# Kernel tuning notes

Measured on AMD Instinct MI355X. Metric: run time of the kernel, lower is better.

The kernel has to match this reference:

```python
import jax, jax.numpy as jnp
import numpy as np

B, H, W = 32768, 28, 28
HID = 800


def dft2(x):
    # centered 2D DFT: fftshift(fft2(ifftshift(x)))
    ax = (-2, -1)
    return jnp.fft.fftshift(jnp.fft.fft2(jnp.fft.ifftshift(x, axes=ax), axes=ax), axes=ax)


def idft2(x):
    ax = (-2, -1)
    return jnp.fft.fftshift(jnp.fft.ifft2(jnp.fft.ifftshift(x, axes=ax), axes=ax), axes=ax)


def setup_inputs() -> dict:
    key = jax.random.key(0)
    k = jax.random.split(key, 5)
    x = jax.random.normal(k[0], (B, H, W), dtype=jnp.float32)
    tmask_re = jnp.ones((1, H, W), dtype=jnp.float32)
    tmask_im = jnp.zeros((1, H, W), dtype=jnp.float32)
    w1 = jax.random.normal(k[1], (HID, H * W), dtype=jnp.float32) * 0.03
    b1 = jax.random.normal(k[2], (HID,), dtype=jnp.float32) * 0.03
    w4 = jax.random.normal(k[3], (10, HID), dtype=jnp.float32) * 0.03
    b4 = jax.random.normal(k[4], (10,), dtype=jnp.float32) * 0.03
    return {"x": x, "tmask_re": tmask_re, "tmask_im": tmask_im,
            "w1": w1, "b1": b1, "w4": w4, "b4": b4}


def reference(x, tmask_re, tmask_im, w1, b1, w4, b4):
    tmask = jax.lax.complex(tmask_re, tmask_im)          # [1,28,28] complex64
    xf = dft2(x.astype(jnp.complex64))                    # [B,28,28] complex64
    xf = tmask * xf                                       # elementwise complex mask
    xr = jnp.real(idft2(xf))                              # back to real image
    h = xr.reshape(-1, H * W)                             # [B,784]
    h = jax.nn.relu(h @ w1.T + b1)                        # [B,800]
    logits = h @ w4.T + b4                                # [B,10]
    return jax.nn.log_softmax(logits, axis=-1)
```

## Files before the change

kernel.cpp:

```cpp
#include <hip/hip_runtime.h>
#include <hip/hip_bf16.h>
#include <cmath>

typedef unsigned short u16;
typedef __attribute__((ext_vector_type(8))) short short8v;
typedef __attribute__((ext_vector_type(4))) unsigned short ushort4v;
typedef __attribute__((ext_vector_type(8))) unsigned short ushort8v;
typedef __attribute__((ext_vector_type(4))) float f32x4;

#define NPIX 784
#define KP   800
#define NH   800
#define STRIDE 808

__device__ __forceinline__ u16 f2bf(float f) {
    union { float f; unsigned int u; } v; v.f = f;
    unsigned int u = v.u;
    unsigned int r = (u + 0x7FFFu + ((u >> 16) & 1u)) >> 16;
    return (u16)r;
}

__global__ void k_kre(const float* __restrict__ MRE, const float* __restrict__ MIM,
                      float* __restrict__ KRE, float* __restrict__ FLAG)
{
    __shared__ float msre[784], msim[784], tre[784], tim[784];
    __shared__ float c28[28], s28[28];
    __shared__ int smax;

    const int t = threadIdx.x;
    if (t < 28) {
        float th = (float)t * (6.283185307179586f / 28.0f);
        s28[t] = sinf(th);
        c28[t] = cosf(th);
    }
    if (t == 0) smax = 0;
    if (t < 784) {
        int r = t / 28, c = t - r * 28;
        int idx = ((r + 14) % 28) * 28 + ((c + 14) % 28);
        msre[t] = MRE[idx];
        msim[t] = MIM[idx];
    }
    __syncthreads();
    if (t < 784) {
        int u = t / 28, cc = t - u * 28;
        float re = 0.f, im = 0.f;
        int ph = 0;
        for (int v = 0; v < 28; ++v) {
            float cr = c28[ph], ci = s28[ph];
            float ar = msre[u * 28 + v], ai = msim[u * 28 + v];
            re += ar * cr - ai * ci;
            im += ar * ci + ai * cr;
            ph += cc; if (ph >= 28) ph -= 28;
        }
        tre[t] = re; tim[t] = im;
    }
    __syncthreads();
    float dev = 0.f;
    if (t < 784) {
        int pr = t / 28, pc = t - pr * 28;
        float s = 0.f;
        int ph = 0;
        for (int u = 0; u < 28; ++u) {
            s += tre[u * 28 + pc] * c28[ph] - tim[u * 28 + pc] * s28[ph];
            ph += pr; if (ph >= 28) ph -= 28;
        }
        s *= (1.0f / 784.0f);
        KRE[t] = s;
        dev = fabsf(s - (t == 0 ? 1.0f : 0.0f));
    }
    #pragma unroll
    for (int m = 32; m >= 1; m >>= 1) dev = fmaxf(dev, __shfl_xor(dev, m, 64));
    if ((t & 63) == 0) atomicMax(&smax, __float_as_int(dev));
    __syncthreads();
    if (t == 0) FLAG[0] = (__int_as_float(smax) < 1e-4f) ? 1.0f : 0.0f;
}

__global__ void k_w1pack(const float* __restrict__ W1, const float* __restrict__ KRE,
                         const float* __restrict__ FLAG, u16* __restrict__ W1P)
{
    const int c = blockIdx.x;
    const int t = threadIdx.x;
    const bool delta = (FLAG[0] > 0.5f);
    __shared__ float w1d[56 * 56];
    __shared__ float kr[784];

    if (delta) {
        if (t < 100) {
            int k0 = t * 8;
            ushort8v h;
            if (k0 + 7 < NPIX) {
                const float4* wp = (const float4*)(W1 + (size_t)c * NPIX + k0);
                float4 a = wp[0], b = wp[1];
                h[0] = f2bf(a.x); h[1] = f2bf(a.y); h[2] = f2bf(a.z); h[3] = f2bf(a.w);
                h[4] = f2bf(b.x); h[5] = f2bf(b.y); h[6] = f2bf(b.z); h[7] = f2bf(b.w);
            } else {
                #pragma unroll
                for (int e = 0; e < 8; ++e) {
                    int k = k0 + e;
                    h[e] = (k < NPIX) ? f2bf(W1[(size_t)c * NPIX + k]) : (u16)0;
                }
            }
            int kf = k0 >> 5, r = k0 & 31;
            int l  = ((r >> 3) << 4) | (c & 15);
            int nf = c >> 4;
            ((ushort8v*)W1P)[(nf * 25 + kf) * 64 + l] = h;
        }
        return;
    }
    for (int i = t; i < 784; i += 128) kr[i] = KRE[i];
    for (int i = t; i < 3136; i += 128) {
        int r = i / 56, cc = i - r * 56;
        w1d[i] = W1[(size_t)c * NPIX + (r % 28) * 28 + (cc % 28)];
    }
    __syncthreads();
    for (int k = t; k < KP; k += 128) {
        float v = 0.f;
        if (k < NPIX) {
            int krr = k / 28, kcc = k - krr * 28;
            for (int dr = 0; dr < 28; ++dr) {
                const float* wrow = &w1d[(krr + dr) * 56 + kcc];
                const float* krow = &kr[dr * 28];
                #pragma unroll 4
                for (int dc = 0; dc < 28; ++dc) v += wrow[dc] * krow[dc];
            }
        }
        int kf = k >> 5, r = k & 31;
        int l  = ((r >> 3) << 4) | (c & 15);
        int nf = c >> 4;
        W1P[(size_t)(((nf * 25 + kf) * 64 + l) << 3) | (r & 7)] = f2bf(v);
    }
}

__global__ void k_w4pack(const float* __restrict__ W4, u16* __restrict__ W4P)
{
    int i = blockIdx.x * 256 + threadIdx.x;
    if (i >= 1600) return;
    int l = i & 63, kt = i >> 6;
    int lc = l & 15, lk = l >> 4;
    ushort8v h;
    #pragma unroll
    for (int e = 0; e < 8; ++e) {
        int k = kt * 32 + lk * 8 + e;
        h[e] = (lc < 10) ? f2bf(W4[lc * NH + k]) : (u16)0;
    }
    ((ushort8v*)W4P)[i] = h;
}

__global__ __launch_bounds__(640) __attribute__((amdgpu_waves_per_eu(3, 3)))
void k_main(
    const float* __restrict__ X, const u16* __restrict__ W1P,
    const u16* __restrict__ W4P, const float* __restrict__ B1,
    const float* __restrict__ B4, float* __restrict__ OUT)
{
    __shared__ __align__(16) u16 As[64 * STRIDE];
    __shared__ __align__(16) float PL2[10 * 4 * 64 * 4];

    const int t = threadIdx.x;
    const int row0 = blockIdx.x * 64;
    const int l = t & 63, w = t >> 6;
    const int lc = l & 15, lk = l >> 4;

    #pragma unroll
    for (int pass = 0; pass < 2; ++pass) {
        float4 y[10];
        #pragma unroll
        for (int i = 0; i < 10; ++i) {
            int idx = t + 640 * (pass * 10 + i);
            int row = idx / 200, q = idx - row * 200;
            if (q < 196)
                y[i] = *(const float4*)(X + (size_t)(row0 + row) * NPIX + (q << 2));
            else
                y[i] = make_float4(0.f, 0.f, 0.f, 0.f);
        }
        #pragma unroll
        for (int i = 0; i < 10; ++i) {
            int idx = t + 640 * (pass * 10 + i);
            int row = idx / 200, q = idx - row * 200;
            ushort4v h;
            h[0] = f2bf(y[i].x); h[1] = f2bf(y[i].y);
            h[2] = f2bf(y[i].z); h[3] = f2bf(y[i].w);
            *(ushort4v*)(As + row * STRIDE + (q << 2)) = h;
        }
    }

    f32x4 acc[4][5];
    #pragma unroll
    for (int m = 0; m < 4; ++m)
        #pragma unroll
        for (int n = 0; n < 5; ++n) acc[m][n] = (f32x4)(0.0f);

    const short8v* BP = (const short8v*)W1P;
    short8v bb[2][5];
    #pragma unroll
    for (int n = 0; n < 5; ++n)
        bb[0][n] = BP[((w * 5 + n) * 25 + 0) * 64 + l];

    __syncthreads();

    #pragma unroll
    for (int kt = 0; kt < 25; ++kt) {
        if (kt < 24) {
            #pragma unroll
            for (int n = 0; n < 5; ++n)
                bb[(kt + 1) & 1][n] = BP[((w * 5 + n) * 25 + (kt + 1)) * 64 + l];
        }
        const u16* ab = As + lc * STRIDE + kt * 32 + lk * 8;
        __builtin_amdgcn_s_setprio(1);
        #pragma unroll
        for (int m = 0; m < 4; ++m) {
            short8v a = *(const short8v*)(ab + m * (16 * STRIDE));
            #pragma unroll
            for (int n = 0; n < 5; ++n)
                acc[m][n] = __builtin_amdgcn_mfma_f32_16x16x32_bf16(a, bb[kt & 1][n], acc[m][n], 0, 0, 0);
        }
        __builtin_amdgcn_s_setprio(0);
    }
    __syncthreads();

    #pragma unroll
    for (int n = 0; n < 5; ++n) {
        float bn = B1[w * 80 + n * 16 + lc];
        #pragma unroll
        for (int m = 0; m < 4; ++m) {
            #pragma unroll
            for (int j = 0; j < 4; ++j) {
                float hv = fmaxf(acc[m][n][j] + bn, 0.0f);
                As[(m * 16 + lk * 4 + j) * STRIDE + (w * 80 + n * 16 + lc)] = f2bf(hv);
            }
        }
    }
    __syncthreads();

    {
        const int ks  = (w < 5) ? 3 * w : 15 + 2 * (w - 5);
        const int cnt = (w < 5) ? 3 : 2;
        const short8v* WP = (const short8v*)W4P;
        f32x4 pc[4];
        #pragma unroll
        for (int m = 0; m < 4; ++m) pc[m] = (f32x4)(0.0f);
        #pragma unroll
        for (int i = 0; i < 3; ++i) {
            if (i < cnt) {
                int kt = ks + i;
                short8v b = WP[kt * 64 + l];
                #pragma unroll
                for (int m = 0; m < 4; ++m) {
                    short8v a = *(const short8v*)(As + (m * 16 + lc) * STRIDE + kt * 32 + lk * 8);
                    pc[m] = __builtin_amdgcn_mfma_f32_16x16x32_bf16(a, b, pc[m], 0, 0, 0);
                }
            }
        }
        f32x4* PLv = (f32x4*)PL2;
        #pragma unroll
        for (int m = 0; m < 4; ++m)
            PLv[(w * 4 + m) * 64 + l] = pc[m];
    }
    __syncthreads();

    if (t < 64) {
        const int r = t;
        const int m = r >> 4, sub = ((r & 15) >> 2) * 16, j = r & 3;
        float lg[10];
        #pragma unroll
        for (int o = 0; o < 10; ++o) {
            float s = B4[o];
            #pragma unroll
            for (int w2 = 0; w2 < 10; ++w2)
                s += PL2[(((w2 * 4 + m) * 64) + sub + o) * 4 + j];
            lg[o] = s;
        }
        float mx = lg[0];
        #pragma unroll
        for (int o = 1; o < 10; ++o) mx = fmaxf(mx, lg[o]);
        float se = 0.f;
        #pragma unroll
        for (int o = 0; o < 10; ++o) se += expf(lg[o] - mx);
        float lse = logf(se);
        float* op = OUT + (size_t)(row0 + r) * 10;
        #pragma unroll
        for (int o = 0; o < 10; ++o) op[o] = lg[o] - mx - lse;
    }
}

extern "C" void kernel_launch(void* const* d_in, const int* in_sizes, int n_in,
                              void* d_out, int out_size, void* d_ws, size_t ws_size,
                              hipStream_t stream)
{
    const float* X   = (const float*)d_in[0];
    const float* MRE = (const float*)d_in[1];
    const float* MIM = (const float*)d_in[2];
    const float* W1  = (const float*)d_in[3];
    const float* B1  = (const float*)d_in[4];
    const float* W4  = (const float*)d_in[5];
    const float* B4  = (const float*)d_in[6];
    float* OUT = (float*)d_out;

    float* kre  = (float*)d_ws;
    float* flag = kre + 784;
    u16*   w1p  = (u16*)((char*)d_ws + 4096);
    u16*   w4p  = (u16*)((char*)d_ws + 4096 + 1310720);

    k_kre<<<1, 832, 0, stream>>>(MRE, MIM, kre, flag);
    k_w1pack<<<800, 128, 0, stream>>>(W1, kre, flag, w1p);
    k_w4pack<<<7, 256, 0, stream>>>(W4, w4p);
    k_main<<<512, 640, 0, stream>>>(X, w1p, w4p, B1, B4, OUT);
}
```

Measured before the change: 71.40 us.

## Overlap X tile loading and bf16 conversion with first-layer MFMA loop

Instead of loading and converting the whole 64x784 input tile to bf16 in shared memory before the GEMM, the kernel now stages it in five column chunks of 160. Each chunk is loaded and converted while MFMAs run on the previous chunk, with a barrier between chunks. The W1 register prefetch is deepened from double to triple buffering, and conversion uses the packed bf16x2 intrinsic. The aim is to hide global load latency of X behind compute, at the cost of four extra barriers and more live registers under a fixed waves-per-EU target.

```diff
diff --git a/kernel.cpp b/kernel.cpp
--- a/kernel.cpp
+++ b/kernel.cpp
@@ -18,6 +18,18 @@
     unsigned int u = v.u;
     unsigned int r = (u + 0x7FFFu + ((u >> 16) & 1u)) >> 16;
     return (u16)r;
+}
+
+__device__ __forceinline__ short8v cvt8(f32x4 v0, f32x4 v1) {
+    union { __hip_bfloat162 h; ushort2 u; } a, b, c, d;
+    a.h = __float22bfloat162_rn(make_float2(v0[0], v0[1]));
+    b.h = __float22bfloat162_rn(make_float2(v0[2], v0[3]));
+    c.h = __float22bfloat162_rn(make_float2(v1[0], v1[1]));
+    d.h = __float22bfloat162_rn(make_float2(v1[2], v1[3]));
+    short8v r;
+    r[0] = (short)a.u.x; r[1] = (short)a.u.y; r[2] = (short)b.u.x; r[3] = (short)b.u.y;
+    r[4] = (short)c.u.x; r[5] = (short)c.u.y; r[6] = (short)d.u.x; r[7] = (short)d.u.y;
+    return r;
 }
 
 __global__ void k_kre(const float* __restrict__ MRE, const float* __restrict__ MIM,
@@ -160,28 +172,9 @@
     const int l = t & 63, w = t >> 6;
     const int lc = l & 15, lk = l >> 4;
 
-    #pragma unroll
-    for (int pass = 0; pass < 2; ++pass) {
-        float4 y[10];
-        #pragma unroll
-        for (int i = 0; i < 10; ++i) {
-            int idx = t + 640 * (pass * 10 + i);
-            int row = idx / 200, q = idx - row * 200;
-            if (q < 196)
-                y[i] = *(const float4*)(X + (size_t)(row0 + row) * NPIX + (q << 2));
-            else
-                y[i] = make_float4(0.f, 0.f, 0.f, 0.f);
-        }
-        #pragma unroll
-        for (int i = 0; i < 10; ++i) {
-            int idx = t + 640 * (pass * 10 + i);
-            int row = idx / 200, q = idx - row * 200;
-            ushort4v h;
-            h[0] = f2bf(y[i].x); h[1] = f2bf(y[i].y);
-            h[2] = f2bf(y[i].z); h[3] = f2bf(y[i].w);
-            *(ushort4v*)(As + row * STRIDE + (q << 2)) = h;
-        }
-    }
+    const int sr = t / 10, sg = t - sr * 10;
+    const float* xs = X + (size_t)(row0 + sr) * NPIX + sg * 16;
+    u16* hw = As + sr * STRIDE + sg * 16;
 
     f32x4 acc[4][5];
     #pragma unroll
@@ -190,30 +183,80 @@
         for (int n = 0; n < 5; ++n) acc[m][n] = (f32x4)(0.0f);
 
     const short8v* BP = (const short8v*)W1P;
-    short8v bb[2][5];
-    #pragma unroll
-    for (int n = 0; n < 5; ++n)
+    short8v bb[3][5];
+    #pragma unroll
+    for (int n = 0; n < 5; ++n) {
         bb[0][n] = BP[((w * 5 + n) * 25 + 0) * 64 + l];
-
-    __syncthreads();
-
-    #pragma unroll
-    for (int kt = 0; kt < 25; ++kt) {
-        if (kt < 24) {
+        bb[1][n] = BP[((w * 5 + n) * 25 + 1) * 64 + l];
+    }
+
+    {
+        f32x4 a0 = *(const f32x4*)(xs);
+        f32x4 a1 = *(const f32x4*)(xs + 4);
+        f32x4 b0 = *(const f32x4*)(xs + 8);
+        f32x4 b1 = *(const f32x4*)(xs + 12);
+        *(short8v*)(hw)     = cvt8(a0, a1);
+        *(short8v*)(hw + 8) = cvt8(b0, b1);
+    }
+    asm volatile("s_waitcnt lgkmcnt(0)" ::: "memory");
+    __builtin_amdgcn_s_barrier();
+    __builtin_amdgcn_sched_barrier(0);
+
+    #pragma unroll
+    for (int c = 0; c < 5; ++c) {
+        const bool st  = (c < 4);
+        const bool pad = (c == 3);
+        const float* xsc = xs + (c + 1) * 160;
+        u16* hwc = hw + (c + 1) * 160;
+        f32x4 ya0, ya1, yb0, yb1;
+
+        if (st && !(pad && sg == 9)) {
+            ya0 = *(const f32x4*)(xsc);
+            ya1 = *(const f32x4*)(xsc + 4);
+        }
+        #pragma unroll
+        for (int kf = 0; kf < 5; ++kf) {
+            const int kt = c * 5 + kf;
+            if (kt < 23) {
+                #pragma unroll
+                for (int n = 0; n < 5; ++n)
+                    bb[(kt + 2) % 3][n] = BP[((w * 5 + n) * 25 + (kt + 2)) * 64 + l];
+            }
+            const u16* ab = As + lc * STRIDE + kt * 32 + lk * 8;
+            __builtin_amdgcn_s_setprio(1);
             #pragma unroll
-            for (int n = 0; n < 5; ++n)
-                bb[(kt + 1) & 1][n] = BP[((w * 5 + n) * 25 + (kt + 1)) * 64 + l];
-        }
-        const u16* ab = As + lc * STRIDE + kt * 32 + lk * 8;
-        __builtin_amdgcn_s_setprio(1);
-        #pragma unroll
-        for (int m = 0; m < 4; ++m) {
-            short8v a = *(const short8v*)(ab + m * (16 * STRIDE));
-            #pragma unroll
-            for (int n = 0; n < 5; ++n)
-                acc[m][n] = __builtin_amdgcn_mfma_f32_16x16x32_bf16(a, bb[kt & 1][n], acc[m][n], 0, 0, 0);
-        }
-        __builtin_amdgcn_s_setprio(0);
+            for (int m = 0; m < 4; ++m) {
+                short8v a = *(const short8v*)(ab + m * (16 * STRIDE));
+                #pragma unroll
+                for (int n = 0; n < 5; ++n)
+                    acc[m][n] = __builtin_amdgcn_mfma_f32_16x16x32_bf16(a, bb[kt % 3][n], acc[m][n], 0, 0, 0);
+            }
+            __builtin_amdgcn_s_setprio(0);
+
+            if (kf == 1 && st) {
+                if (pad && sg == 9) {
+                    short8v z = (short8v)(0);
+                    *(short8v*)(hwc) = z;
+                } else {
+                    *(short8v*)(hwc) = cvt8(ya0, ya1);
+                    yb0 = *(const f32x4*)(xsc + 8);
+                    yb1 = *(const f32x4*)(xsc + 12);
+                }
+            }
+            if (kf == 3 && st) {
+                if (pad && sg == 9) {
+                    short8v z = (short8v)(0);
+                    *(short8v*)(hwc + 8) = z;
+                } else {
+                    *(short8v*)(hwc + 8) = cvt8(yb0, yb1);
+                }
+            }
+        }
+        if (c < 4) {
+            asm volatile("s_waitcnt lgkmcnt(0)" ::: "memory");
+            __builtin_amdgcn_s_barrier();
+            __builtin_amdgcn_sched_barrier(0);
+        }
     }
     __syncthreads();
 
```

New measurement: 121.7 us. 70.4% more time.
